# Performance work log

Measured on AMD Instinct MI355X. Metric: run time of the kernel, lower is better.

Reference implementation:

```python
import jax, jax.numpy as jnp
import numpy as np

HIDDEN = 1024
FEAT = 2048
BOTTLENECK = 512
B, T = 64, 512


def setup_inputs() -> dict:
    key = jax.random.key(0)
    k1, k2, k3, k4, k5 = jax.random.split(key, 5)
    hidden = jax.random.normal(k1, (B, HIDDEN), dtype=jnp.float32)
    feats = jax.random.normal(k2, (B, T, FEAT), dtype=jnp.float32)
    # nn.Linear weights stored as [out, in]; apply as x @ W.T
    W = jax.random.normal(k3, (BOTTLENECK, HIDDEN), dtype=jnp.float32) * (1.0 / np.sqrt(HIDDEN))
    U = jax.random.normal(k4, (BOTTLENECK, FEAT), dtype=jnp.float32) * (1.0 / np.sqrt(FEAT))
    b = jnp.ones((BOTTLENECK,), dtype=jnp.float32)
    w = jax.random.normal(k5, (1, BOTTLENECK), dtype=jnp.float32) * (1.0 / np.sqrt(BOTTLENECK))
    return {"hidden": hidden, "feats": feats, "W": W, "U": U, "b": b, "w": w}


def reference(hidden, feats, W, U, b, w):
    Wh = hidden @ W.T                      # [B, K]
    Uv = jnp.einsum('btf,kf->btk', feats, U)  # [B, T, K]
    e = jnp.tanh(Wh[:, None, :] + Uv + b)  # [B, T, K]
    energies = jnp.einsum('btk,ok->bto', e, w)  # [B, T, 1]
    weights = jax.nn.softmax(energies, axis=1)  # softmax over time
    attn_feats = jnp.sum(feats * weights, axis=1)  # [B, F]
    return attn_feats, weights
```

## Files before the change

kernel.cpp:

```cpp
#include <hip/hip_runtime.h>
#include <hip/hip_bf16.h>
#include <math.h>

#define BATCH 64
#define TDIM 512
#define FEAT 2048
#define HID 1024
#define KDIM 512
#define MROWS (BATCH * TDIM)
#define TCH 8
#define TCLEN (TDIM / TCH)

typedef __attribute__((ext_vector_type(8))) short short8;
typedef __attribute__((ext_vector_type(4))) float floatx4;

#define GLL16(g, l)                                                     \
    __builtin_amdgcn_global_load_lds(                                   \
        (const __attribute__((address_space(1))) void*)(g),             \
        (__attribute__((address_space(3))) void*)(l), 16, 0, 0)

__device__ __forceinline__ unsigned short f2bf(float x) {
    unsigned int u = __float_as_uint(x);
    u += 0x7FFFu + ((u >> 16) & 1u);
    return (unsigned short)(u >> 16);
}

__global__ __launch_bounds__(256) void k_convert(const float* __restrict__ src,
                                                 unsigned short* __restrict__ dst,
                                                 int n4) {
    int stride = gridDim.x * blockDim.x;
    for (int i = blockIdx.x * blockDim.x + threadIdx.x; i < n4; i += stride) {
        float4 v = ((const float4*)src)[i];
        ushort4 o;
        o.x = f2bf(v.x); o.y = f2bf(v.y); o.z = f2bf(v.z); o.w = f2bf(v.w);
        ((ushort4*)dst)[i] = o;
    }
}

__global__ __launch_bounds__(256) void k1_whb(const float* __restrict__ hidden,
                                              const float* __restrict__ W,
                                              const float* __restrict__ bias,
                                              float* __restrict__ whb) {
    int b = blockIdx.y;
    int k = blockIdx.x * 4 + (threadIdx.x >> 6);
    int lane = threadIdx.x & 63;
    const float* hrow = hidden + (size_t)b * HID;
    const float* wrow = W + (size_t)k * HID;
    float acc = 0.f;
    #pragma unroll 4
    for (int h = lane; h < HID; h += 64) acc += hrow[h] * wrow[h];
    #pragma unroll
    for (int off = 32; off > 0; off >>= 1) acc += __shfl_down(acc, off, 64);
    if (lane == 0) whb[b * KDIM + k] = acc + bias[k];
}

__global__ __launch_bounds__(256) void k2_mfma(const unsigned short* __restrict__ fB,
                                               const unsigned short* __restrict__ uB,
                                               const float* __restrict__ whb,
                                               const float* __restrict__ wvec,
                                               float* __restrict__ partial) {
    __shared__ unsigned short As[128 * 32];
    __shared__ unsigned short Bs[128 * 32];
    __shared__ float sums[2][128];

    const int tid  = threadIdx.x;
    const int wave = tid >> 6;
    const int lane = tid & 63;
    const int row0 = blockIdx.x * 128;
    const int k0   = blockIdx.y * 128;
    const int wm = wave >> 1, wn = wave & 1;
    const int col = lane & 15, quad = lane >> 4;

    const int c0 = wave * 128 + lane;
    const int c1 = c0 + 64;
    const int r0c = c0 >> 2, r1c = c1 >> 2;
    const int q0 = (c0 & 3) ^ ((r0c >> 1) & 3);
    const int q1 = (c1 & 3) ^ ((r1c >> 1) & 3);
    const unsigned short* gA0 = fB + (size_t)(row0 + r0c) * FEAT + q0 * 8;
    const unsigned short* gA1 = fB + (size_t)(row0 + r1c) * FEAT + q1 * 8;
    const unsigned short* gB0 = uB + (size_t)(k0 + r0c) * FEAT + q0 * 8;
    const unsigned short* gB1 = uB + (size_t)(k0 + r1c) * FEAT + q1 * 8;
    unsigned short* lA0 = As + wave * 1024;
    unsigned short* lA1 = lA0 + 512;
    unsigned short* lB0 = Bs + wave * 1024;
    unsigned short* lB1 = lB0 + 512;

    const int sw = (quad ^ ((col >> 1) & 3)) * 8;

    floatx4 acc[4][4];
    #pragma unroll
    for (int i = 0; i < 4; ++i)
        #pragma unroll
        for (int j = 0; j < 4; ++j) acc[i][j] = (floatx4){0.f, 0.f, 0.f, 0.f};

    for (int f0 = 0; f0 < FEAT; f0 += 32) {
        GLL16(gA0, lA0); GLL16(gA1, lA1);
        GLL16(gB0, lB0); GLL16(gB1, lB1);
        gA0 += 32; gA1 += 32; gB0 += 32; gB1 += 32;
        __syncthreads();

        short8 af[4], bf[4];
        #pragma unroll
        for (int i = 0; i < 4; ++i)
            af[i] = *(const short8*)&As[(wm * 64 + i * 16 + col) * 32 + sw];
        #pragma unroll
        for (int j = 0; j < 4; ++j)
            bf[j] = *(const short8*)&Bs[(wn * 64 + j * 16 + col) * 32 + sw];
        #pragma unroll
        for (int i = 0; i < 4; ++i)
            #pragma unroll
            for (int j = 0; j < 4; ++j)
                acc[i][j] = __builtin_amdgcn_mfma_f32_16x16x32_bf16(
                    af[i], bf[j], acc[i][j], 0, 0, 0);
        __syncthreads();
    }

    const int b = row0 >> 9;
    float wk[4], hk[4];
    #pragma unroll
    for (int j = 0; j < 4; ++j) {
        int k = k0 + wn * 64 + j * 16 + col;
        wk[j] = wvec[k];
        hk[j] = whb[b * KDIM + k];
    }
    #pragma unroll
    for (int i = 0; i < 4; ++i) {
        #pragma unroll
        for (int r = 0; r < 4; ++r) {
            float s = 0.f;
            #pragma unroll
            for (int j = 0; j < 4; ++j)
                s += tanhf(acc[i][j][r] + hk[j]) * wk[j];
            #pragma unroll
            for (int off = 8; off > 0; off >>= 1)
                s += __shfl_down(s, off, 16);
            if (col == 0)
                sums[wn][wm * 64 + i * 16 + quad * 4 + r] = s;
        }
    }
    __syncthreads();
    if (tid < 128)
        partial[blockIdx.y * MROWS + row0 + tid] = sums[0][tid] + sums[1][tid];
}

#define BM 128
#define BN 128
#define BF 16
#define LDSPAD 4

__global__ __launch_bounds__(256) void k2_energy(const float* __restrict__ feats,
                                                 const float* __restrict__ U,
                                                 const float* __restrict__ whb,
                                                 const float* __restrict__ wvec,
                                                 float* __restrict__ partial) {
    __shared__ __align__(16) float As[BF][BM + LDSPAD];
    __shared__ __align__(16) float Us[BF][BN + LDSPAD];

    const int row0 = blockIdx.x * BM;
    const int k0   = blockIdx.y * BN;
    const int tid  = threadIdx.x;
    const int tx   = tid & 15;
    const int ty   = tid >> 4;

    float acc[8][8];
    #pragma unroll
    for (int i = 0; i < 8; ++i)
        #pragma unroll
        for (int j = 0; j < 8; ++j) acc[i][j] = 0.f;

    for (int f0 = 0; f0 < FEAT; f0 += BF) {
        #pragma unroll
        for (int l = 0; l < 2; ++l) {
            int li = tid + l * 256;
            int r  = li >> 2;
            int c4 = (li & 3) * 4;
            float4 av = *(const float4*)(feats + (size_t)(row0 + r) * FEAT + f0 + c4);
            float4 uv = *(const float4*)(U     + (size_t)(k0   + r) * FEAT + f0 + c4);
            As[c4 + 0][r] = av.x; As[c4 + 1][r] = av.y;
            As[c4 + 2][r] = av.z; As[c4 + 3][r] = av.w;
            Us[c4 + 0][r] = uv.x; Us[c4 + 1][r] = uv.y;
            Us[c4 + 2][r] = uv.z; Us[c4 + 3][r] = uv.w;
        }
        __syncthreads();
        #pragma unroll
        for (int kf = 0; kf < BF; ++kf) {
            float4 a0 = *(const float4*)&As[kf][ty * 8];
            float4 a1 = *(const float4*)&As[kf][ty * 8 + 4];
            float4 u0 = *(const float4*)&Us[kf][tx * 8];
            float4 u1 = *(const float4*)&Us[kf][tx * 8 + 4];
            float a[8] = {a0.x, a0.y, a0.z, a0.w, a1.x, a1.y, a1.z, a1.w};
            float u[8] = {u0.x, u0.y, u0.z, u0.w, u1.x, u1.y, u1.z, u1.w};
            #pragma unroll
            for (int i = 0; i < 8; ++i)
                #pragma unroll
                for (int j = 0; j < 8; ++j) acc[i][j] += a[i] * u[j];
        }
        __syncthreads();
    }

    const int b = row0 >> 9;
    float psum[8];
    #pragma unroll
    for (int i = 0; i < 8; ++i) {
        float s = 0.f;
        #pragma unroll
        for (int j = 0; j < 8; ++j) {
            int k = k0 + tx * 8 + j;
            s += tanhf(acc[i][j] + whb[b * KDIM + k]) * wvec[k];
        }
        psum[i] = s;
    }
    #pragma unroll
    for (int off = 8; off > 0; off >>= 1)
        #pragma unroll
        for (int i = 0; i < 8; ++i) psum[i] += __shfl_down(psum[i], off, 16);

    if (tx == 0) {
        int c = blockIdx.y;
        #pragma unroll
        for (int i = 0; i < 8; ++i)
            partial[c * MROWS + row0 + ty * 8 + i] = psum[i];
    }
}

__global__ __launch_bounds__(512) void k3_softmax(const float* __restrict__ partial,
                                                  float* __restrict__ wout) {
    int b = blockIdx.x;
    int t = threadIdx.x;
    float e = 0.f;
    #pragma unroll
    for (int c = 0; c < 4; ++c) e += partial[c * MROWS + b * TDIM + t];

    __shared__ float sm[512];
    sm[t] = e;
    __syncthreads();
    #pragma unroll
    for (int s = 256; s > 0; s >>= 1) {
        if (t < s) sm[t] = fmaxf(sm[t], sm[t + s]);
        __syncthreads();
    }
    float m = sm[0];
    __syncthreads();
    float ex = __expf(e - m);
    sm[t] = ex;
    __syncthreads();
    #pragma unroll
    for (int s = 256; s > 0; s >>= 1) {
        if (t < s) sm[t] += sm[t + s];
        __syncthreads();
    }
    float inv = 1.f / sm[0];
    wout[b * TDIM + t] = ex * inv;
}

__global__ __launch_bounds__(256) void k4_partial(const float* __restrict__ feats,
                                                  const float* __restrict__ weights,
                                                  float* __restrict__ partial4) {
    int b  = blockIdx.z;
    int t0 = blockIdx.y * TCLEN;
    int f4 = (blockIdx.x * 256 + threadIdx.x) * 4;
    __shared__ float wsm[TCLEN];
    if (threadIdx.x < TCLEN) wsm[threadIdx.x] = weights[b * TDIM + t0 + threadIdx.x];
    __syncthreads();

    const float* fp = feats + (size_t)b * TDIM * FEAT + (size_t)t0 * FEAT + f4;
    float ax = 0.f, ay = 0.f, az = 0.f, aw = 0.f;
    float bx = 0.f, by = 0.f, bz = 0.f, bw = 0.f;
    #pragma unroll 4
    for (int t = 0; t < TCLEN; t += 4) {
        float4 v0 = *(const float4*)(fp + (size_t)(t + 0) * FEAT);
        float4 v1 = *(const float4*)(fp + (size_t)(t + 1) * FEAT);
        float4 v2 = *(const float4*)(fp + (size_t)(t + 2) * FEAT);
        float4 v3 = *(const float4*)(fp + (size_t)(t + 3) * FEAT);
        float w0 = wsm[t], w1 = wsm[t + 1], w2 = wsm[t + 2], w3 = wsm[t + 3];
        ax += v0.x * w0; ay += v0.y * w0; az += v0.z * w0; aw += v0.w * w0;
        bx += v1.x * w1; by += v1.y * w1; bz += v1.z * w1; bw += v1.w * w1;
        ax += v2.x * w2; ay += v2.y * w2; az += v2.z * w2; aw += v2.w * w2;
        bx += v3.x * w3; by += v3.y * w3; bz += v3.z * w3; bw += v3.w * w3;
    }
    float4 o;
    o.x = ax + bx; o.y = ay + by; o.z = az + bz; o.w = aw + bw;
    *(float4*)(partial4 + ((size_t)blockIdx.y * BATCH + b) * FEAT + f4) = o;
}

__global__ __launch_bounds__(256) void k5_reduce(const float* __restrict__ partial4,
                                                 float* __restrict__ out) {
    int i4 = blockIdx.x * 256 + threadIdx.x;
    float4 s = ((const float4*)partial4)[i4];
    #pragma unroll
    for (int c = 1; c < TCH; ++c) {
        float4 v = ((const float4*)partial4)[(size_t)c * (BATCH * FEAT / 4) + i4];
        s.x += v.x; s.y += v.y; s.z += v.z; s.w += v.w;
    }
    ((float4*)out)[i4] = s;
}

__global__ __launch_bounds__(256) void k4_direct(const float* __restrict__ feats,
                                                 const float* __restrict__ weights,
                                                 float* __restrict__ out) {
    int b = blockIdx.y;
    int f4 = (blockIdx.x * 256 + threadIdx.x) * 4;
    __shared__ float wsm[TDIM];
    wsm[threadIdx.x]       = weights[b * TDIM + threadIdx.x];
    wsm[threadIdx.x + 256] = weights[b * TDIM + 256 + threadIdx.x];
    __syncthreads();

    const float* fp = feats + (size_t)b * TDIM * FEAT + f4;
    float ax = 0.f, ay = 0.f, az = 0.f, aw = 0.f;
    for (int t = 0; t < TDIM; ++t) {
        float4 v = *(const float4*)(fp + (size_t)t * FEAT);
        float w = wsm[t];
        ax += v.x * w; ay += v.y * w; az += v.z * w; aw += v.w * w;
    }
    float4 o = {ax, ay, az, aw};
    *(float4*)(out + (size_t)b * FEAT + f4) = o;
}

extern "C" void kernel_launch(void* const* d_in, const int* in_sizes, int n_in,
                              void* d_out, int out_size, void* d_ws, size_t ws_size,
                              hipStream_t stream) {
    const float* hidden = (const float*)d_in[0];
    const float* feats  = (const float*)d_in[1];
    const float* W      = (const float*)d_in[2];
    const float* U      = (const float*)d_in[3];
    const float* bias   = (const float*)d_in[4];
    const float* wvec   = (const float*)d_in[5];

    float* out         = (float*)d_out;
    float* attn_out    = out;
    float* weights_out = out + (size_t)BATCH * FEAT;
    float* whb         = weights_out;
    float* partial     = attn_out;

    const size_t featsN = (size_t)MROWS * FEAT;
    const size_t uN     = (size_t)KDIM * FEAT;
    const size_t bf16Bytes = (featsN + uN) * sizeof(unsigned short);
    const size_t poolBytes = (size_t)TCH * BATCH * FEAT * sizeof(float);
    const bool fast = ws_size >= bf16Bytes + poolBytes;

    k1_whb<<<dim3(KDIM / 4, BATCH), 256, 0, stream>>>(hidden, W, bias, whb);

    if (fast) {
        unsigned short* fBf = (unsigned short*)d_ws;
        unsigned short* uBf = fBf + featsN;
        float* pool4 = (float*)((char*)d_ws + bf16Bytes);
        k_convert<<<1024, 256, 0, stream>>>(feats, fBf, (int)(featsN / 4));
        k_convert<<<256, 256, 0, stream>>>(U, uBf, (int)(uN / 4));
        k2_mfma<<<dim3(MROWS / 128, KDIM / 128), 256, 0, stream>>>(
            fBf, uBf, whb, wvec, partial);
        k3_softmax<<<dim3(BATCH), 512, 0, stream>>>(partial, weights_out);
        k4_partial<<<dim3(FEAT / 1024, TCH, BATCH), 256, 0, stream>>>(
            feats, weights_out, pool4);
        k5_reduce<<<dim3(BATCH * FEAT / 4 / 256), 256, 0, stream>>>(pool4, attn_out);
    } else {
        k2_energy<<<dim3(MROWS / 128, KDIM / 128), 256, 0, stream>>>(
            feats, U, whb, wvec, partial);
        k3_softmax<<<dim3(BATCH), 512, 0, stream>>>(partial, weights_out);
        k4_direct<<<dim3(FEAT / 1024, BATCH), 256, 0, stream>>>(
            feats, weights_out, attn_out);
    }
}
```

Measured before the change: 555.2 us.

## Enlarge MFMA GEMM tile to 256 rows, merge bf16 converts, double pooling chunks

Result: no change. 547.1 us (-1.5%).

```diff
diff --git a/kernel.cpp b/kernel.cpp
--- a/kernel.cpp
+++ b/kernel.cpp
@@ -8,7 +8,7 @@
 #define HID 1024
 #define KDIM 512
 #define MROWS (BATCH * TDIM)
-#define TCH 8
+#define TCH 16
 #define TCLEN (TDIM / TCH)
 
 typedef __attribute__((ext_vector_type(8))) short short8;
@@ -25,15 +25,21 @@
     return (unsigned short)(u >> 16);
 }
 
-__global__ __launch_bounds__(256) void k_convert(const float* __restrict__ src,
-                                                 unsigned short* __restrict__ dst,
-                                                 int n4) {
+__global__ __launch_bounds__(256) void k_convert2(const float* __restrict__ feats,
+                                                  const float* __restrict__ U,
+                                                  unsigned short* __restrict__ fB,
+                                                  unsigned short* __restrict__ uB,
+                                                  int n4f, int n4tot) {
     int stride = gridDim.x * blockDim.x;
-    for (int i = blockIdx.x * blockDim.x + threadIdx.x; i < n4; i += stride) {
-        float4 v = ((const float4*)src)[i];
+    for (int i = blockIdx.x * blockDim.x + threadIdx.x; i < n4tot; i += stride) {
+        const float4* src = (i < n4f) ? (const float4*)feats + i
+                                      : (const float4*)U + (i - n4f);
+        ushort4* dst = (i < n4f) ? (ushort4*)fB + i
+                                 : (ushort4*)uB + (i - n4f);
+        float4 v = *src;
         ushort4 o;
         o.x = f2bf(v.x); o.y = f2bf(v.y); o.z = f2bf(v.z); o.w = f2bf(v.w);
-        ((ushort4*)dst)[i] = o;
+        *dst = o;
     }
 }
 
@@ -54,60 +60,68 @@
     if (lane == 0) whb[b * KDIM + k] = acc + bias[k];
 }
 
-__global__ __launch_bounds__(256) void k2_mfma(const unsigned short* __restrict__ fB,
-                                               const unsigned short* __restrict__ uB,
-                                               const float* __restrict__ whb,
-                                               const float* __restrict__ wvec,
-                                               float* __restrict__ partial) {
-    __shared__ unsigned short As[128 * 32];
+__global__ __launch_bounds__(256, 2) void k2_mfma(const unsigned short* __restrict__ fB,
+                                                  const unsigned short* __restrict__ uB,
+                                                  const float* __restrict__ whb,
+                                                  const float* __restrict__ wvec,
+                                                  float* __restrict__ partial) {
+    __shared__ unsigned short As[256 * 32];
     __shared__ unsigned short Bs[128 * 32];
-    __shared__ float sums[2][128];
+    __shared__ float sums[2][256];
 
     const int tid  = threadIdx.x;
     const int wave = tid >> 6;
     const int lane = tid & 63;
-    const int row0 = blockIdx.x * 128;
+    const int row0 = blockIdx.x * 256;
     const int k0   = blockIdx.y * 128;
     const int wm = wave >> 1, wn = wave & 1;
     const int col = lane & 15, quad = lane >> 4;
 
-    const int c0 = wave * 128 + lane;
-    const int c1 = c0 + 64;
-    const int r0c = c0 >> 2, r1c = c1 >> 2;
-    const int q0 = (c0 & 3) ^ ((r0c >> 1) & 3);
-    const int q1 = (c1 & 3) ^ ((r1c >> 1) & 3);
-    const unsigned short* gA0 = fB + (size_t)(row0 + r0c) * FEAT + q0 * 8;
-    const unsigned short* gA1 = fB + (size_t)(row0 + r1c) * FEAT + q1 * 8;
-    const unsigned short* gB0 = uB + (size_t)(k0 + r0c) * FEAT + q0 * 8;
-    const unsigned short* gB1 = uB + (size_t)(k0 + r1c) * FEAT + q1 * 8;
-    unsigned short* lA0 = As + wave * 1024;
-    unsigned short* lA1 = lA0 + 512;
-    unsigned short* lB0 = Bs + wave * 1024;
-    unsigned short* lB1 = lB0 + 512;
+    const unsigned short* gA[4];
+    unsigned short* lA[4];
+    #pragma unroll
+    for (int g = 0; g < 4; ++g) {
+        int s = wave * 256 + g * 64 + lane;
+        int r = s >> 2;
+        int q = (s & 3) ^ ((r >> 1) & 3);
+        gA[g] = fB + (size_t)(row0 + r) * FEAT + q * 8;
+        lA[g] = As + (wave * 256 + g * 64) * 8;
+    }
+    const unsigned short* gBp[2];
+    unsigned short* lB[2];
+    #pragma unroll
+    for (int g = 0; g < 2; ++g) {
+        int s = wave * 128 + g * 64 + lane;
+        int r = s >> 2;
+        int q = (s & 3) ^ ((r >> 1) & 3);
+        gBp[g] = uB + (size_t)(k0 + r) * FEAT + q * 8;
+        lB[g] = Bs + (wave * 128 + g * 64) * 8;
+    }
 
     const int sw = (quad ^ ((col >> 1) & 3)) * 8;
 
-    floatx4 acc[4][4];
-    #pragma unroll
-    for (int i = 0; i < 4; ++i)
+    floatx4 acc[8][4];
+    #pragma unroll
+    for (int i = 0; i < 8; ++i)
         #pragma unroll
         for (int j = 0; j < 4; ++j) acc[i][j] = (floatx4){0.f, 0.f, 0.f, 0.f};
 
     for (int f0 = 0; f0 < FEAT; f0 += 32) {
-        GLL16(gA0, lA0); GLL16(gA1, lA1);
-        GLL16(gB0, lB0); GLL16(gB1, lB1);
-        gA0 += 32; gA1 += 32; gB0 += 32; gB1 += 32;
-        __syncthreads();
-
-        short8 af[4], bf[4];
-        #pragma unroll
-        for (int i = 0; i < 4; ++i)
-            af[i] = *(const short8*)&As[(wm * 64 + i * 16 + col) * 32 + sw];
+        #pragma unroll
+        for (int g = 0; g < 4; ++g) { GLL16(gA[g], lA[g]); gA[g] += 32; }
+        #pragma unroll
+        for (int g = 0; g < 2; ++g) { GLL16(gBp[g], lB[g]); gBp[g] += 32; }
+        __syncthreads();
+
+        short8 af[8], bf[4];
+        #pragma unroll
+        for (int i = 0; i < 8; ++i)
+            af[i] = *(const short8*)&As[(wm * 128 + i * 16 + col) * 32 + sw];
         #pragma unroll
         for (int j = 0; j < 4; ++j)
             bf[j] = *(const short8*)&Bs[(wn * 64 + j * 16 + col) * 32 + sw];
         #pragma unroll
-        for (int i = 0; i < 4; ++i)
+        for (int i = 0; i < 8; ++i)
             #pragma unroll
             for (int j = 0; j < 4; ++j)
                 acc[i][j] = __builtin_amdgcn_mfma_f32_16x16x32_bf16(
@@ -124,7 +138,7 @@
         hk[j] = whb[b * KDIM + k];
     }
     #pragma unroll
-    for (int i = 0; i < 4; ++i) {
+    for (int i = 0; i < 8; ++i) {
         #pragma unroll
         for (int r = 0; r < 4; ++r) {
             float s = 0.f;
@@ -135,12 +149,11 @@
             for (int off = 8; off > 0; off >>= 1)
                 s += __shfl_down(s, off, 16);
             if (col == 0)
-                sums[wn][wm * 64 + i * 16 + quad * 4 + r] = s;
+                sums[wn][wm * 128 + i * 16 + quad * 4 + r] = s;
         }
     }
     __syncthreads();
-    if (tid < 128)
-        partial[blockIdx.y * MROWS + row0 + tid] = sums[0][tid] + sums[1][tid];
+    partial[blockIdx.y * MROWS + row0 + tid] = sums[0][tid] + sums[1][tid];
 }
 
 #define BM 128
@@ -344,9 +357,10 @@
         unsigned short* fBf = (unsigned short*)d_ws;
         unsigned short* uBf = fBf + featsN;
         float* pool4 = (float*)((char*)d_ws + bf16Bytes);
-        k_convert<<<1024, 256, 0, stream>>>(feats, fBf, (int)(featsN / 4));
-        k_convert<<<256, 256, 0, stream>>>(U, uBf, (int)(uN / 4));
-        k2_mfma<<<dim3(MROWS / 128, KDIM / 128), 256, 0, stream>>>(
+        k_convert2<<<1024, 256, 0, stream>>>(feats, U, fBf, uBf,
+                                             (int)(featsN / 4),
+                                             (int)((featsN + uN) / 4));
+        k2_mfma<<<dim3(MROWS / 256, KDIM / 128), 256, 0, stream>>>(
             fBf, uBf, whb, wvec, partial);
         k3_softmax<<<dim3(BATCH), 512, 0, stream>>>(partial, weights_out);
         k4_partial<<<dim3(FEAT / 1024, TCH, BATCH), 256, 0, stream>>>(
```
